# Optimization experiments

Hardware: AMD Instinct MI355X
Metric: run time of the kernel (lower is better)

The kernel has to match this reference:

```python
import jax, jax.numpy as jnp
import numpy as np

B, T, D, H, K = 8, 512, 768, 8, 4
HD = D // H
SCALE = 1.0 / float(np.sqrt(HD))
EPS = 1e-5


def _ln(x, g, b):
    m = jnp.mean(x, -1, keepdims=True)
    v = jnp.mean((x - m) ** 2, -1, keepdims=True)
    return (x - m) * jax.lax.rsqrt(v + EPS) * g + b


def _attn(q, k, v, mask=None):
    # q,k,v: [B,T,D] -> multi-head scaled dot product, returns [B,T,D]
    sp = lambda t: t.reshape(B, T, H, HD).transpose(0, 2, 1, 3)  # [B,H,T,hd]
    a = jnp.einsum('bhqd,bhkd->bhqk', sp(q), sp(k)) * SCALE
    if mask is not None:
        a = jnp.where(mask, -jnp.inf, a)
    a = jax.nn.softmax(a, -1)
    o = jnp.einsum('bhqk,bhkd->bhqd', a, sp(v))
    return o.transpose(0, 2, 1, 3).reshape(B, T, D)


def setup_inputs() -> dict:
    key = jax.random.key(0)
    ks = iter(jax.random.split(key, 20))
    n = lambda shp: jax.random.normal(next(ks), shp, jnp.float32) * 0.02
    z = lambda shp: jnp.zeros(shp, jnp.float32)
    o = lambda shp: jnp.ones(shp, jnp.float32)
    return dict(
        x=jax.random.normal(next(ks), (B, T, D), jnp.float32),
        router_w1=n((128, D)), router_b1=z((128,)),
        router_w2=n((2 * K, 128)), router_b2=z((2 * K,)),
        norm_s_g=o((D,)), norm_s_b=z((D,)),
        norm_t_g=o((D,)), norm_t_b=z((D,)),
        norm_mlp_g=o((D,)), norm_mlp_b=z((D,)),
        sp_wqkv=n((K, 3 * D, D)), sp_bqkv=z((K, 3 * D)),
        sp_wo=n((K, D, D)), sp_bo=z((K, D)),
        tp_wq=n((K, D, D)), tp_bq=z((K, D)),
        tp_wk=n((K, D, D)), tp_bk=z((K, D)),
        tp_wv=n((K, D, D)), tp_bv=z((K, D)),
        tp_wo=n((K, D, D)), tp_bo=z((K, D)),
        cross_wqkv=n((3 * D, D)), cross_bqkv=z((3 * D,)),
        cross_wo=n((D, D)), cross_bo=z((D,)),
        mlp_w1=n((4 * D, D)), mlp_b1=z((4 * D,)),
        mlp_w2=n((D, 4 * D)), mlp_b2=z((D,)),
    )


def _forward(x, router_w1, router_b1, router_w2, router_b2,
             norm_s_g, norm_s_b, norm_t_g, norm_t_b, norm_mlp_g, norm_mlp_b,
             sp_wqkv, sp_bqkv, sp_wo, sp_bo,
             tp_wq, tp_bq, tp_wk, tp_bk, tp_wv, tp_bv, tp_wo, tp_bo,
             cross_wqkv, cross_bqkv, cross_wo, cross_bo,
             mlp_w1, mlp_b1, mlp_w2, mlp_b2):
    # --- router: top-1 expert per sample for each branch ---
    h = jax.nn.gelu(x.mean(1) @ router_w1.T + router_b1, approximate=False)
    route = jax.nn.softmax(h @ router_w2.T + router_b2, -1)  # [B, 2K]
    idx_s = jnp.argmax(route[:, :K], -1)  # [B] top-1 spatial expert
    idx_t = jnp.argmax(route[:, K:], -1)  # [B] top-1 temporal expert

    # --- spatial branch: per-sample routed MultiheadAttention (self-attn) ---
    xn = _ln(x, norm_s_g, norm_s_b)
    qkv = jnp.einsum('btd,bed->bte', xn, sp_wqkv[idx_s]) + sp_bqkv[idx_s][:, None, :]
    q, k, v = jnp.split(qkv, 3, -1)
    so = _attn(q, k, v)
    spatial_out = jnp.einsum('btd,bed->bte', so, sp_wo[idx_s]) + sp_bo[idx_s][:, None, :]

    # --- temporal branch: per-sample routed causal attention (with residual) ---
    xt = _ln(x, norm_t_g, norm_t_b)
    qt = jnp.einsum('btd,bed->bte', xt, tp_wq[idx_t]) + tp_bq[idx_t][:, None, :]
    kt = jnp.einsum('btd,bed->bte', xt, tp_wk[idx_t]) + tp_bk[idx_t][:, None, :]
    vt = jnp.einsum('btd,bed->bte', xt, tp_wv[idx_t]) + tp_bv[idx_t][:, None, :]
    causal = jnp.triu(jnp.ones((T, T), bool), 1)
    to = _attn(qt, kt, vt, mask=causal)
    to = jnp.einsum('btd,bed->bte', to, tp_wo[idx_t]) + tp_bo[idx_t][:, None, :]
    temporal_out = xt + to  # CausalTimeAttention2 adds residual to its (normed) query

    # --- cross attention fusing the two branches ---
    cq = spatial_out @ cross_wqkv[:D].T + cross_bqkv[:D]
    ck = temporal_out @ cross_wqkv[D:2 * D].T + cross_bqkv[D:2 * D]
    cv = temporal_out @ cross_wqkv[2 * D:].T + cross_bqkv[2 * D:]
    fused = _attn(cq, ck, cv) @ cross_wo.T + cross_bo

    x = x + fused
    y = jax.nn.gelu(_ln(x, norm_mlp_g, norm_mlp_b) @ mlp_w1.T + mlp_b1, approximate=False)
    x = x + (y @ mlp_w2.T + mlp_b2)
    return x


def reference(x, router_w1, router_b1, router_w2, router_b2,
              norm_s_g, norm_s_b, norm_t_g, norm_t_b, norm_mlp_g, norm_mlp_b,
              sp_wqkv, sp_bqkv, sp_wo, sp_bo,
              tp_wq, tp_bq, tp_wk, tp_bk, tp_wv, tp_bv, tp_wo, tp_bo,
              cross_wqkv, cross_bqkv, cross_wo, cross_bo,
              mlp_w1, mlp_b1, mlp_w2, mlp_b2):
    return _forward(x, router_w1, router_b1, router_w2, router_b2,
                    norm_s_g, norm_s_b, norm_t_g, norm_t_b, norm_mlp_g, norm_mlp_b,
                    sp_wqkv, sp_bqkv, sp_wo, sp_bo,
                    tp_wq, tp_bq, tp_wk, tp_bk, tp_wv, tp_bv, tp_wo, tp_bo,
                    cross_wqkv, cross_bqkv, cross_wo, cross_bo,
                    mlp_w1, mlp_b1, mlp_w2, mlp_b2)
```

## Files before the change

### kernel.cpp

```cpp
#include <hip/hip_runtime.h>
#include <math.h>

#define BB 8
#define TT 512
#define DD 768
#define HH 8
#define HDIM 96
#define DDDD 589824LL

typedef short s16x8 __attribute__((ext_vector_type(8)));
typedef float f32x4 __attribute__((ext_vector_type(4)));
typedef unsigned short u16;

__device__ inline unsigned short f2bf(float f) {
    union { float f; unsigned u; } v; v.f = f;
    unsigned u = v.u;
    unsigned r = (u + 0x7fffu + ((u >> 16) & 1u)) >> 16;
    return (unsigned short)r;
}

__device__ inline float bf2f(u16 h) {
    union { unsigned u; float f; } v; v.u = ((unsigned)h) << 16; return v.f;
}

__device__ inline float gelu_exact(float x) {
    return 0.5f * x * (1.0f + erff(x * 0.70710678118654752440f));
}

__device__ __forceinline__ void gload16(const void* g, void* l) {
    __builtin_amdgcn_global_load_lds(
        (const __attribute__((address_space(1))) unsigned int*)g,
        (__attribute__((address_space(3))) unsigned int*)l,
        16, 0, 0);
}

__device__ __forceinline__ long long tix(int m, int k, int ldn) {
    return ((long long)(m >> 6) * (ldn >> 3) + (k >> 3)) * 512 + ((m & 63) << 3) + (k & 7);
}

#define CUM1  7077888LL
#define CUM2  9437184LL
#define CUM3  11796480LL
#define CUM4  14155776LL
#define CUM5  16515072LL
#define CUM6  18874368LL
#define CUM7  20643840LL
#define CUM8  21233664LL
#define CUM9  23592960LL
#define CUM10 25952256LL

__global__ __launch_bounds__(256) void cvt_kernel(
    const float* __restrict__ s0, const float* __restrict__ s1,
    const float* __restrict__ s2, const float* __restrict__ s3,
    const float* __restrict__ s4, const float* __restrict__ s5,
    const float* __restrict__ s6, const float* __restrict__ s7,
    const float* __restrict__ s8, const float* __restrict__ s9,
    u16* __restrict__ dpool)
{
    long long g = ((long long)blockIdx.x * 256 + threadIdx.x) * 8;
    if (g >= CUM10) return;
    const float* s; long long i, base; int n, k, K = 768;
    const long long SZQKV = 2304LL * 768;
    if (g < CUM1) {
        s = s0; i = g;
        long long e = i / SZQKV, r = i - e * SZQKV;
        n = (int)(r / 768); k = (int)(r % 768); base = e * 3 * DDDD;
    } else if (g < CUM2) {
        s = s1; i = g - CUM1;
        long long e = i / DDDD, r = i - e * DDDD;
        n = (int)(r / 768); k = (int)(r % 768); base = CUM1 + e * DDDD;
    } else if (g < CUM5) {
        int tp = (g < CUM3) ? 0 : (g < CUM4) ? 1 : 2;
        s = (tp == 0) ? s2 : (tp == 1) ? s3 : s4;
        i = g - ((tp == 0) ? CUM2 : (tp == 1) ? CUM3 : CUM4);
        long long e = i / DDDD, r = i - e * DDDD;
        n = tp * 768 + (int)(r / 768); k = (int)(r % 768);
        base = CUM2 + e * 3 * DDDD;
    } else if (g < CUM6) {
        s = s5; i = g - CUM5;
        long long e = i / DDDD, r = i - e * DDDD;
        n = (int)(r / 768); k = (int)(r % 768); base = CUM5 + e * DDDD;
    } else if (g < CUM7) {
        s = s6; i = g - CUM6;
        n = (int)(i / 768); k = (int)(i % 768); base = CUM6;
    } else if (g < CUM8) {
        s = s7; i = g - CUM7;
        n = (int)(i / 768); k = (int)(i % 768); base = CUM7;
    } else if (g < CUM9) {
        s = s8; i = g - CUM8;
        n = (int)(i / 768); k = (int)(i % 768); base = CUM8;
    } else {
        s = s9; i = g - CUM9;
        n = (int)(i / 3072); k = (int)(i % 3072); base = CUM9; K = 3072;
    }
    float4 a = *(const float4*)(s + i);
    float4 b = *(const float4*)(s + i + 4);
    s16x8 o;
    o[0] = f2bf(a.x); o[1] = f2bf(a.y); o[2] = f2bf(a.z); o[3] = f2bf(a.w);
    o[4] = f2bf(b.x); o[5] = f2bf(b.y); o[6] = f2bf(b.z); o[7] = f2bf(b.w);
    long long d = base + (((long long)(n >> 7) * (K >> 3) + (k >> 3)) << 10) + ((n & 127) << 3);
    *(s16x8*)(dpool + d) = o;
}

__global__ __launch_bounds__(256) void pack_tpb_kernel(
    const float* __restrict__ bq, const float* __restrict__ bk,
    const float* __restrict__ bv, float* __restrict__ dst)
{
    int t = blockIdx.x * 256 + threadIdx.x;
    if (t >= 4 * 2304) return;
    int e = t / 2304, n = t - e * 2304;
    float v = (n < 768) ? bq[e * 768 + n]
            : (n < 1536) ? bk[e * 768 + n - 768]
            : bv[e * 768 + n - 1536];
    dst[t] = v;
}

#define SLABA 2048
#define SLABB 4096

template<int OUT_MODE, int RES_MODE>
__global__ __launch_bounds__(256) void gemm_bf16_kernel(
    const u16* __restrict__ A, long long sAb,
    const u16* __restrict__ B, const int* __restrict__ bidx, long long sBexp,
    void* __restrict__ Cv, long long sCb, int ldc,
    const float* __restrict__ bias, long long sBiasExp,
    const void* __restrict__ residv, long long sResB, int ldr,
    int act, int N, int K)
{
    int zb = blockIdx.z;
    int kw8 = K >> 3;
    const u16* Ab = A + zb * sAb + (long long)blockIdx.y * kw8 * 512;
    const u16* Bb = B + (bidx ? (long long)bidx[zb] * sBexp : 0)
                      + (long long)blockIdx.x * kw8 * 1024;
    const float* biasb = bias ? (bias + (bidx ? (long long)bidx[zb] * sBiasExp : 0)) : nullptr;

    __shared__ __align__(16) u16 As[4][SLABA];
    __shared__ __align__(16) u16 Bs[4][SLABB];

    int tid = threadIdx.x;
    int wave = tid >> 6, lane = tid & 63;
    int wr = wave >> 1, wc = wave & 1;
    int lrow = lane & 15, lkg = lane >> 4;

    f32x4 acc[2][4];
    #pragma unroll
    for (int i = 0; i < 2; i++)
        #pragma unroll
        for (int j = 0; j < 4; j++)
            acc[i][j] = (f32x4){0.f, 0.f, 0.f, 0.f};

    const u16* agt = Ab + tid * 8;
    const u16* bgt = Bb + tid * 8;
    u16* al  = (u16*)As + tid * 8;
    u16* bl0 = (u16*)Bs + tid * 8;
    u16* bl1 = (u16*)Bs + (tid + 256) * 8;

    auto stage = [&](int slab, int buf) {
        gload16(agt + slab * SLABA,        al  + buf * SLABA);
        gload16(bgt + slab * SLABB,        bl0 + buf * SLABB);
        gload16(bgt + slab * SLABB + 2048, bl1 + buf * SLABB);
    };

    int nK = K >> 5;
    stage(0, 0);
    stage(1, 1);
    stage(2, 2);

    for (int kt = 0; kt < nK; ++kt) {
        if (kt + 2 < nK)      asm volatile("s_waitcnt vmcnt(6)" ::: "memory");
        else if (kt + 1 < nK) asm volatile("s_waitcnt vmcnt(3)" ::: "memory");
        else                  asm volatile("s_waitcnt vmcnt(0)" ::: "memory");
        __builtin_amdgcn_s_barrier();
        __builtin_amdgcn_sched_barrier(0);
        if (kt + 3 < nK) stage(kt + 3, (kt + 3) & 3);

        const u16* Asb = &As[kt & 3][0];
        const u16* Bsb = &Bs[kt & 3][0];
        s16x8 af[2], bf[4];
        #pragma unroll
        for (int i = 0; i < 2; ++i)
            af[i] = *(const s16x8*)&Asb[((lkg) * 64 + wr * 32 + i * 16 + lrow) * 8];
        #pragma unroll
        for (int j = 0; j < 4; ++j)
            bf[j] = *(const s16x8*)&Bsb[((lkg) * 128 + wc * 64 + j * 16 + lrow) * 8];
        #pragma unroll
        for (int i = 0; i < 2; ++i)
            #pragma unroll
            for (int j = 0; j < 4; ++j)
                acc[i][j] = __builtin_amdgcn_mfma_f32_16x16x32_bf16(af[i], bf[j], acc[i][j], 0, 0, 0);
    }

    int n0 = blockIdx.x * 128;
    int m0 = blockIdx.y * 64;
    float* Cf = (float*)Cv + zb * sCb;
    u16* Ch = (u16*)Cv + zb * sCb;
    const float* Rf = (const float*)residv + zb * sResB;
    const u16* Rh = (const u16*)residv + zb * sResB;
    int col16 = lane & 15;
    int rq = (lane >> 4) * 4;
    #pragma unroll
    for (int j = 0; j < 4; ++j) {
        int n = n0 + wc * 64 + j * 16 + col16;
        float bv = biasb ? biasb[n] : 0.0f;
        #pragma unroll
        for (int i = 0; i < 2; ++i) {
            #pragma unroll
            for (int r = 0; r < 4; ++r) {
                int m = m0 + wr * 32 + i * 16 + rq + r;
                float v = acc[i][j][r] + bv;
                if (act == 1) v = gelu_exact(v);
                if (RES_MODE == 1) v += Rf[(long long)m * ldr + n];
                if (RES_MODE == 2) v += bf2f(Rh[tix(m, n, ldr)]);
                if (OUT_MODE == 0) Cf[(long long)m * ldc + n] = v;
                if (OUT_MODE == 1) Ch[(long long)m * ldc + n] = f2bf(v);
                if (OUT_MODE == 2) Ch[tix(m, n, ldc)] = f2bf(v);
            }
        }
    }
}

__global__ __launch_bounds__(256, 2) void attn_kernel(
    const u16* __restrict__ QKV, u16* __restrict__ Out,
    int causal, float scale)
{
    int qt = blockIdx.x;
    int bh = blockIdx.y;
    int b = bh >> 3;
    int h = bh & 7;
    const u16* Qb = QKV + (long long)b * TT * 3 * DD + (long long)h * HDIM;
    const u16* Kb = Qb + DD;
    const u16* Vb = Qb + 2 * DD;
    u16* Ob = Out + (long long)b * TT * DD;

    __shared__ __align__(16) u16 Qs[64 * 104];
    __shared__ __align__(16) u16 Ks[64 * 104];
    __shared__ __align__(16) u16 Vs[96 * 72];
    __shared__ __align__(16) u16 Ps[64 * 72];

    int tid = threadIdx.x;
    int wave = tid >> 6;
    int lane = tid & 63;
    int col16 = lane & 15;
    int lkg = lane >> 4;
    int lk = lkg * 8;
    int m0 = qt * 64;

    #pragma unroll
    for (int it = 0; it < 3; ++it) {
        int s = tid + it * 256;
        int r = s / 12, c8 = (s % 12) * 8;
        *(s16x8*)&Qs[r * 104 + c8] = *(const s16x8*)(Qb + (long long)(m0 + r) * (3 * DD) + c8);
    }
    __syncthreads();

    s16x8 qf[3];
    #pragma unroll
    for (int kk = 0; kk < 3; ++kk)
        qf[kk] = *(const s16x8*)&Qs[(wave * 16 + col16) * 104 + kk * 32 + lk];

    f32x4 acc[32];
    #pragma unroll
    for (int n = 0; n < 32; ++n) acc[n] = (f32x4){0.f, 0.f, 0.f, 0.f};

    #pragma unroll
    for (int kt = 0; kt < 8; ++kt) {
        #pragma unroll
        for (int it = 0; it < 3; ++it) {
            int s = tid + it * 256;
            int r = s / 12, c8 = (s % 12) * 8;
            *(s16x8*)&Ks[r * 104 + c8] = *(const s16x8*)(Kb + (long long)(kt * 64 + r) * (3 * DD) + c8);
        }
        __syncthreads();
        #pragma unroll
        for (int kk = 0; kk < 3; ++kk) {
            #pragma unroll
            for (int j = 0; j < 4; ++j) {
                s16x8 bfr = *(const s16x8*)&Ks[(j * 16 + col16) * 104 + kk * 32 + lk];
                acc[kt * 4 + j] = __builtin_amdgcn_mfma_f32_16x16x32_bf16(qf[kk], bfr, acc[kt * 4 + j], 0, 0, 0);
            }
        }
        __syncthreads();
    }

    int rowbase = m0 + wave * 16 + lkg * 4;
    float mx[4];
    #pragma unroll
    for (int r = 0; r < 4; ++r) mx[r] = -3.0e38f;
    #pragma unroll
    for (int n = 0; n < 32; ++n) {
        int colg = n * 16 + col16;
        #pragma unroll
        for (int r = 0; r < 4; ++r) {
            float v = acc[n][r] * scale;
            if (causal && colg > rowbase + r) v = -3.0e38f;
            acc[n][r] = v;
            mx[r] = fmaxf(mx[r], v);
        }
    }
    #pragma unroll
    for (int m = 1; m <= 8; m <<= 1)
        #pragma unroll
        for (int r = 0; r < 4; ++r)
            mx[r] = fmaxf(mx[r], __shfl_xor(mx[r], m, 64));

    float sum[4] = {0.f, 0.f, 0.f, 0.f};
    #pragma unroll
    for (int n = 0; n < 32; ++n) {
        #pragma unroll
        for (int r = 0; r < 4; ++r) {
            float e = __expf(acc[n][r] - mx[r]);
            acc[n][r] = e;
            sum[r] += e;
        }
    }
    #pragma unroll
    for (int m = 1; m <= 8; m <<= 1)
        #pragma unroll
        for (int r = 0; r < 4; ++r)
            sum[r] += __shfl_xor(sum[r], m, 64);
    float inv[4];
    #pragma unroll
    for (int r = 0; r < 4; ++r) inv[r] = 1.0f / sum[r];

    f32x4 oacc[6];
    #pragma unroll
    for (int j = 0; j < 6; ++j) oacc[j] = (f32x4){0.f, 0.f, 0.f, 0.f};

    #pragma unroll
    for (int kt = 0; kt < 8; ++kt) {
        __syncthreads();
        #pragma unroll
        for (int j = 0; j < 4; ++j) {
            #pragma unroll
            for (int r = 0; r < 4; ++r)
                Ps[(wave * 16 + lkg * 4 + r) * 72 + j * 16 + col16] = f2bf(acc[kt * 4 + j][r]);
        }
        #pragma unroll
        for (int it = 0; it < 3; ++it) {
            int s = tid + it * 256;
            int key = s / 12, c8 = (s % 12) * 8;
            s16x8 v = *(const s16x8*)(Vb + (long long)(kt * 64 + key) * (3 * DD) + c8);
            #pragma unroll
            for (int e = 0; e < 8; ++e)
                Vs[(c8 + e) * 72 + key] = (u16)v[e];
        }
        __syncthreads();
        #pragma unroll
        for (int kk = 0; kk < 2; ++kk) {
            s16x8 pf = *(const s16x8*)&Ps[(wave * 16 + col16) * 72 + kk * 32 + lk];
            #pragma unroll
            for (int j = 0; j < 6; ++j) {
                s16x8 vf = *(const s16x8*)&Vs[(j * 16 + col16) * 72 + kk * 32 + lk];
                oacc[j] = __builtin_amdgcn_mfma_f32_16x16x32_bf16(pf, vf, oacc[j], 0, 0, 0);
            }
        }
    }

    int rquad = lkg * 4;
    #pragma unroll
    for (int j = 0; j < 6; ++j) {
        int d = h * 96 + j * 16 + col16;
        #pragma unroll
        for (int r = 0; r < 4; ++r) {
            int row = m0 + wave * 16 + rquad + r;
            Ob[tix(row, d, DD)] = f2bf(oacc[j][r] * inv[r]);
        }
    }
}

__global__ __launch_bounds__(256) void ln_kernel(
    const float* __restrict__ x, const float* __restrict__ g,
    const float* __restrict__ b, u16* __restrict__ out)
{
    long long row = blockIdx.x;
    const float* xr = x + row * DD;
    u16* ob = out + (row >> 9) * ((long long)TT * DD);
    int m = (int)(row & 511);
    int t = threadIdx.x;
    float vals[3];
    float s = 0.f, ss = 0.f;
    #pragma unroll
    for (int i = 0; i < 3; i++) {
        float v = xr[t + i * 256];
        vals[i] = v; s += v; ss += v * v;
    }
    __shared__ float rs[256], rss[256];
    rs[t] = s; rss[t] = ss; __syncthreads();
    for (int k = 128; k > 0; k >>= 1) {
        if (t < k) { rs[t] += rs[t + k]; rss[t] += rss[t + k]; }
        __syncthreads();
    }
    float mean = rs[0] * (1.0f / DD);
    float var = rss[0] * (1.0f / DD) - mean * mean;
    float inv = rsqrtf(var + 1e-5f);
    #pragma unroll
    for (int i = 0; i < 3; i++) {
        int d = t + i * 256;
        ob[tix(m, d, DD)] = f2bf((vals[i] - mean) * inv * g[d] + b[d]);
    }
}

__global__ __launch_bounds__(256) void mean_part_kernel(
    const float* __restrict__ x, float* __restrict__ part)
{
    int b = blockIdx.x, dseg = blockIdx.y, rc = blockIdx.z;
    int d = dseg * 256 + threadIdx.x;
    const float* xb = x + (long long)b * TT * DD;
    float s = 0.f;
    int r0 = rc * 64;
    for (int r = r0; r < r0 + 64; ++r) s += xb[(long long)r * DD + d];
    part[((long long)b * 8 + rc) * DD + d] = s;
}

__global__ __launch_bounds__(128) void router_kernel(
    const float* __restrict__ part, const float* __restrict__ w1,
    const float* __restrict__ b1, const float* __restrict__ w2,
    const float* __restrict__ b2, int* __restrict__ idx)
{
    int b = blockIdx.x, t = threadIdx.x;
    __shared__ float xm[DD];
    __shared__ float h[128];
    __shared__ float logits[8];
    for (int i = t; i < DD; i += 128) {
        float s = 0.f;
        for (int rc = 0; rc < 8; ++rc) s += part[((long long)b * 8 + rc) * DD + i];
        xm[i] = s * (1.0f / TT);
    }
    __syncthreads();
    {
        float s = b1[t];
        const float* w = w1 + (long long)t * DD;
        for (int d = 0; d < DD; ++d) s += xm[d] * w[d];
        h[t] = gelu_exact(s);
    }
    __syncthreads();
    if (t < 8) {
        float s = b2[t];
        const float* w = w2 + t * 128;
        for (int d = 0; d < 128; ++d) s += h[d] * w[d];
        logits[t] = s;
    }
    __syncthreads();
    if (t == 0) {
        int bsix = 0;
        for (int i = 1; i < 4; i++) if (logits[i] > logits[bsix]) bsix = i;
        int btix = 4;
        for (int i = 5; i < 8; i++) if (logits[i] > logits[btix]) btix = i;
        idx[b] = bsix;
        idx[b + BB] = btix - 4;
    }
}

static void run_gemm2(hipStream_t stream,
    const u16* A, long long sAb,
    const u16* B, const int* bidx, long long sBexp,
    void* C, long long sCb, int ldc,
    const float* bias, long long sBiasExp,
    const void* resid, long long sResB, int ldr,
    int act, int N, int K, int outmode, int resmode)
{
    dim3 grid(N / 128, 8, BB);
    if (outmode == 1)
        gemm_bf16_kernel<1, 0><<<grid, 256, 0, stream>>>(A, sAb, B, bidx, sBexp,
            C, sCb, ldc, bias, sBiasExp, resid, sResB, ldr, act, N, K);
    else if (outmode == 2 && resmode == 0)
        gemm_bf16_kernel<2, 0><<<grid, 256, 0, stream>>>(A, sAb, B, bidx, sBexp,
            C, sCb, ldc, bias, sBiasExp, resid, sResB, ldr, act, N, K);
    else if (outmode == 2)
        gemm_bf16_kernel<2, 2><<<grid, 256, 0, stream>>>(A, sAb, B, bidx, sBexp,
            C, sCb, ldc, bias, sBiasExp, resid, sResB, ldr, act, N, K);
    else
        gemm_bf16_kernel<0, 1><<<grid, 256, 0, stream>>>(A, sAb, B, bidx, sBexp,
            C, sCb, ldc, bias, sBiasExp, resid, sResB, ldr, act, N, K);
}

extern "C" void kernel_launch(void* const* d_in, const int* in_sizes, int n_in,
                              void* d_out, int out_size, void* d_ws, size_t ws_size,
                              hipStream_t stream)
{
    const float* x       = (const float*)d_in[0];
    const float* rw1     = (const float*)d_in[1];
    const float* rb1     = (const float*)d_in[2];
    const float* rw2     = (const float*)d_in[3];
    const float* rb2     = (const float*)d_in[4];
    const float* gs      = (const float*)d_in[5];
    const float* bs      = (const float*)d_in[6];
    const float* gt      = (const float*)d_in[7];
    const float* btt     = (const float*)d_in[8];
    const float* gm      = (const float*)d_in[9];
    const float* bm      = (const float*)d_in[10];
    const float* sp_wqkv = (const float*)d_in[11];
    const float* sp_bqkv = (const float*)d_in[12];
    const float* sp_wo   = (const float*)d_in[13];
    const float* sp_bo   = (const float*)d_in[14];
    const float* tp_wq   = (const float*)d_in[15];
    const float* tp_bq   = (const float*)d_in[16];
    const float* tp_wk   = (const float*)d_in[17];
    const float* tp_bk   = (const float*)d_in[18];
    const float* tp_wv   = (const float*)d_in[19];
    const float* tp_bv   = (const float*)d_in[20];
    const float* tp_wo   = (const float*)d_in[21];
    const float* tp_bo   = (const float*)d_in[22];
    const float* c_wqkv  = (const float*)d_in[23];
    const float* c_bqkv  = (const float*)d_in[24];
    const float* c_wo    = (const float*)d_in[25];
    const float* c_bo    = (const float*)d_in[26];
    const float* m_w1    = (const float*)d_in[27];
    const float* m_b1    = (const float*)d_in[28];
    const float* m_w2    = (const float*)d_in[29];
    const float* m_b2    = (const float*)d_in[30];
    float* out = (float*)d_out;

    float* ws = (float*)d_ws;
    size_t o = 0;
    float* part  = ws + o; o += (size_t)BB * 8 * DD;
    int*   idx   = (int*)(ws + o); o += 16;
    float* tpb   = ws + o; o += 4 * 2304;
    float* x1b   = ws + o; o += (size_t)4096 * DD;
    u16* xnb   = (u16*)(ws + o); o += (size_t)4096 * DD / 2;
    u16* tmp1b = (u16*)(ws + o); o += (size_t)4096 * DD / 2;
    u16* tmp2b = (u16*)(ws + o); o += (size_t)4096 * DD / 2;
    u16* soutb = (u16*)(ws + o); o += (size_t)4096 * DD / 2;
    u16* toutb = (u16*)(ws + o); o += (size_t)4096 * DD / 2;
    u16* qkvb  = (u16*)(ws + o); o += (size_t)4096 * 2304 / 2;
    u16* yb    = (u16*)(ws + o); o += (size_t)4096 * 3072 / 2;
    u16* wpool = (u16*)(ws + o); o += (size_t)CUM10 / 2;

    u16* w_sp_qkv = wpool;
    u16* w_sp_wo  = wpool + CUM1;
    u16* w_tp_qkv = wpool + CUM2;
    u16* w_tp_o   = wpool + CUM5;
    u16* w_c_qkv  = wpool + CUM6;
    u16* w_c_wo   = wpool + CUM7;
    u16* w_m1     = wpool + CUM8;
    u16* w_m2     = wpool + CUM9;

    int* idx_s = idx;
    int* idx_t = idx + BB;

    const long long sTD  = (long long)TT * DD;
    const long long sT3D = (long long)TT * 3 * DD;
    const long long sT4D = (long long)TT * 4 * DD;
    const float qk_scale = 1.0f / sqrtf((float)HDIM);

    cvt_kernel<<<(int)((CUM10 / 8 + 255) / 256), 256, 0, stream>>>(
        sp_wqkv, sp_wo, tp_wq, tp_wk, tp_wv, tp_wo, c_wqkv, c_wo, m_w1, m_w2, wpool);
    pack_tpb_kernel<<<36, 256, 0, stream>>>(tp_bq, tp_bk, tp_bv, tpb);

    mean_part_kernel<<<dim3(BB, 3, 8), 256, 0, stream>>>(x, part);
    router_kernel<<<BB, 128, 0, stream>>>(part, rw1, rb1, rw2, rb2, idx);

    ln_kernel<<<4096, 256, 0, stream>>>(x, gs, bs, xnb);
    run_gemm2(stream, xnb, sTD, w_sp_qkv, idx_s, 3 * DDDD,
              qkvb, sT3D, 3 * DD, sp_bqkv, 3 * DD, nullptr, 0, 0,
              0, 3 * DD, DD, 1, 0);
    attn_kernel<<<dim3(TT / 64, BB * HH), 256, 0, stream>>>(qkvb, tmp1b, 0, qk_scale);
    run_gemm2(stream, tmp1b, sTD, w_sp_wo, idx_s, DDDD,
              soutb, sTD, DD, sp_bo, DD, nullptr, 0, 0,
              0, DD, DD, 2, 0);

    ln_kernel<<<4096, 256, 0, stream>>>(x, gt, btt, xnb);
    run_gemm2(stream, xnb, sTD, w_tp_qkv, idx_t, 3 * DDDD,
              qkvb, sT3D, 3 * DD, tpb, 3 * DD, nullptr, 0, 0,
              0, 3 * DD, DD, 1, 0);
    attn_kernel<<<dim3(TT / 64, BB * HH), 256, 0, stream>>>(qkvb, tmp1b, 1, qk_scale);
    run_gemm2(stream, tmp1b, sTD, w_tp_o, idx_t, DDDD,
              toutb, sTD, DD, tp_bo, DD, xnb, sTD, DD,
              0, DD, DD, 2, 2);

    run_gemm2(stream, soutb, sTD, w_c_qkv, nullptr, 0,
              qkvb, sT3D, 3 * DD, c_bqkv, 0, nullptr, 0, 0,
              0, DD, DD, 1, 0);
    run_gemm2(stream, toutb, sTD, w_c_qkv + DDDD, nullptr, 0,
              qkvb + DD, sT3D, 3 * DD, c_bqkv + DD, 0, nullptr, 0, 0,
              0, 2 * DD, DD, 1, 0);
    attn_kernel<<<dim3(TT / 64, BB * HH), 256, 0, stream>>>(qkvb, tmp1b, 0, qk_scale);
    run_gemm2(stream, tmp1b, sTD, w_c_wo, nullptr, 0,
              x1b, sTD, DD, c_bo, 0, x, sTD, DD,
              0, DD, DD, 0, 1);

    ln_kernel<<<4096, 256, 0, stream>>>(x1b, gm, bm, tmp2b);
    run_gemm2(stream, tmp2b, sTD, w_m1, nullptr, 0,
              yb, sT4D, 4 * DD, m_b1, 0, nullptr, 0, 0,
              1, 4 * DD, DD, 2, 0);
    run_gemm2(stream, yb, sT4D, w_m2, nullptr, 0,
              out, sTD, DD, m_b2, 0, x1b, sTD, DD,
              0, DD, 4 * DD, 0, 1);
}
```

Before: 694.4 us.

## Deepen GEMM LDS pipeline to six stages and remap blocks across XCDs

```diff
diff --git a/kernel.cpp b/kernel.cpp
--- a/kernel.cpp
+++ b/kernel.cpp
@@ -127,15 +127,23 @@
     const void* __restrict__ residv, long long sResB, int ldr,
     int act, int N, int K)
 {
-    int zb = blockIdx.z;
+    int nbx = gridDim.x, nby = gridDim.y;
+    int nblk = nbx * nby * (int)gridDim.z;
+    int lin = blockIdx.x + nbx * (blockIdx.y + nby * blockIdx.z);
+    int q = nblk >> 3, r = nblk & 7;
+    int xcd = lin & 7, pos = lin >> 3;
+    int nl = (xcd < r ? xcd * (q + 1) : r * (q + 1) + (xcd - r) * q) + pos;
+    int bx = nl % nbx; int t1 = nl / nbx; int by = t1 % nby; int bz = t1 / nby;
+
+    int zb = bz;
     int kw8 = K >> 3;
-    const u16* Ab = A + zb * sAb + (long long)blockIdx.y * kw8 * 512;
+    const u16* Ab = A + zb * sAb + (long long)by * kw8 * 512;
     const u16* Bb = B + (bidx ? (long long)bidx[zb] * sBexp : 0)
-                      + (long long)blockIdx.x * kw8 * 1024;
+                      + (long long)bx * kw8 * 1024;
     const float* biasb = bias ? (bias + (bidx ? (long long)bidx[zb] * sBiasExp : 0)) : nullptr;
 
-    __shared__ __align__(16) u16 As[4][SLABA];
-    __shared__ __align__(16) u16 Bs[4][SLABB];
+    __shared__ __align__(16) u16 As[6][SLABA];
+    __shared__ __align__(16) u16 Bs[6][SLABB];
 
     int tid = threadIdx.x;
     int wave = tid >> 6, lane = tid & 63;
@@ -162,20 +170,24 @@
     };
 
     int nK = K >> 5;
-    stage(0, 0);
-    stage(1, 1);
-    stage(2, 2);
-
+    stage(0, 0); stage(1, 1); stage(2, 2); stage(3, 3); stage(4, 4);
+
+    int cur = 0, nxt = 5;
     for (int kt = 0; kt < nK; ++kt) {
-        if (kt + 2 < nK)      asm volatile("s_waitcnt vmcnt(6)" ::: "memory");
-        else if (kt + 1 < nK) asm volatile("s_waitcnt vmcnt(3)" ::: "memory");
-        else                  asm volatile("s_waitcnt vmcnt(0)" ::: "memory");
+        int infl = nK - 1 - kt; if (infl > 4) infl = 4;
+        switch (infl) {
+            case 4: asm volatile("s_waitcnt vmcnt(12)" ::: "memory"); break;
+            case 3: asm volatile("s_waitcnt vmcnt(9)" ::: "memory"); break;
+            case 2: asm volatile("s_waitcnt vmcnt(6)" ::: "memory"); break;
+            case 1: asm volatile("s_waitcnt vmcnt(3)" ::: "memory"); break;
+            default: asm volatile("s_waitcnt vmcnt(0)" ::: "memory"); break;
+        }
         __builtin_amdgcn_s_barrier();
         __builtin_amdgcn_sched_barrier(0);
-        if (kt + 3 < nK) stage(kt + 3, (kt + 3) & 3);
-
-        const u16* Asb = &As[kt & 3][0];
-        const u16* Bsb = &Bs[kt & 3][0];
+        if (kt + 5 < nK) stage(kt + 5, nxt);
+
+        const u16* Asb = &As[cur][0];
+        const u16* Bsb = &Bs[cur][0];
         s16x8 af[2], bf[4];
         #pragma unroll
         for (int i = 0; i < 2; ++i)
@@ -188,10 +200,12 @@
             #pragma unroll
             for (int j = 0; j < 4; ++j)
                 acc[i][j] = __builtin_amdgcn_mfma_f32_16x16x32_bf16(af[i], bf[j], acc[i][j], 0, 0, 0);
-    }
-
-    int n0 = blockIdx.x * 128;
-    int m0 = blockIdx.y * 64;
+        cur = (cur + 1 == 6) ? 0 : cur + 1;
+        nxt = (nxt + 1 == 6) ? 0 : nxt + 1;
+    }
+
+    int n0 = bx * 128;
+    int m0 = by * 64;
     float* Cf = (float*)Cv + zb * sCb;
     u16* Ch = (u16*)Cv + zb * sCb;
     const float* Rf = (const float*)residv + zb * sResB;
@@ -205,9 +219,9 @@
         #pragma unroll
         for (int i = 0; i < 2; ++i) {
             #pragma unroll
-            for (int r = 0; r < 4; ++r) {
-                int m = m0 + wr * 32 + i * 16 + rq + r;
-                float v = acc[i][j][r] + bv;
+            for (int r2 = 0; r2 < 4; ++r2) {
+                int m = m0 + wr * 32 + i * 16 + rq + r2;
+                float v = acc[i][j][r2] + bv;
                 if (act == 1) v = gelu_exact(v);
                 if (RES_MODE == 1) v += Rf[(long long)m * ldr + n];
                 if (RES_MODE == 2) v += bf2f(Rh[tix(m, n, ldr)]);
```

New measurement: 738.5 us. 1.06x slower.
